# Kernel tuning notes

Hardware: AMD Instinct MI355X
Metric: run time of the kernel (lower is better)

The kernel has to match this reference:

```python
import jax, jax.numpy as jnp
import numpy as np

NUM_HEADS = 12
NUM_PATCHES = 4096
DIM = 768
IN_DIMS = DIM // NUM_HEADS
SCALE = NUM_PATCHES ** (-0.5)
LN_EPS = 1e-5


def setup_inputs() -> dict:
    key = jax.random.key(0)
    ks = jax.random.split(key, 14)
    s = 0.02
    return {
        "x": jax.random.normal(ks[0], (16, NUM_PATCHES, DIM), dtype=jnp.float32),
        "wq": jax.random.normal(ks[1], (DIM, DIM), dtype=jnp.float32) * s,
        "bq": jnp.zeros((DIM,), dtype=jnp.float32),
        "wk": jax.random.normal(ks[2], (DIM, DIM), dtype=jnp.float32) * s,
        "bk": jnp.zeros((DIM,), dtype=jnp.float32),
        "w_g": jax.random.normal(ks[3], (NUM_PATCHES,), dtype=jnp.float32),
        "w_fc": jax.random.normal(ks[4], (IN_DIMS, DIM), dtype=jnp.float32) * s,
        "b_fc": jnp.zeros((DIM,), dtype=jnp.float32),
        "w_fc2": jax.random.normal(ks[5], (NUM_HEADS, NUM_HEADS), dtype=jnp.float32) * s,
        "b_fc2": jnp.zeros((NUM_HEADS,), dtype=jnp.float32),
        "w_proj": jax.random.normal(ks[6], (DIM, DIM), dtype=jnp.float32) * s,
        "b_proj": jnp.zeros((DIM,), dtype=jnp.float32),
        "gamma": jnp.ones((DIM,), dtype=jnp.float32),
        "beta": jnp.zeros((DIM,), dtype=jnp.float32),
    }


def layernorm(x, gamma, beta):
    mu = jnp.mean(x, axis=-1, keepdims=True)
    var = jnp.mean(jnp.square(x - mu), axis=-1, keepdims=True)
    return (x - mu) * jax.lax.rsqrt(var + LN_EPS) * gamma + beta


def reference(x, wq, bq, wk, bk, w_g, w_fc, b_fc, w_fc2, b_fc2, w_proj, b_proj, gamma, beta):
    bs, n, d = x.shape
    q = x @ wq + bq                      # (b,n,d)  fc_q
    k = x @ wk + bk                      # (b,n,d)  fc_k (reassigned x in torch)
    # query_weight = (q^T @ w_g)^T -> (b,1,d); softmax over channel dim
    qw = jnp.einsum("bnd,n->bd", q, w_g) * SCALE
    A = jax.nn.softmax(qw, axis=-1)      # (b,d)
    # G = sum_n(A * k): A is constant over n, so equals A * sum_n k
    G = A * jnp.sum(k, axis=1)           # (b,d)
    # sigmoid gating chain on pooled q
    dv = jnp.mean(q, axis=1)             # (b,d)   AdaptiveAvgPool over n
    dv = dv.reshape(bs, NUM_HEADS, IN_DIMS)
    dv = jax.nn.gelu(dv @ w_fc + b_fc, approximate=False)   # (b,H,d)
    dv = dv.reshape(bs, d, NUM_HEADS)    # reshape (not transpose), as in torch
    dv = dv @ w_fc2 + b_fc2              # (b,d,H)
    dv = jax.nn.sigmoid(jnp.mean(dv, axis=-1))               # (b,d)
    G = G * dv                           # (b,d)
    out = (G[:, None, :] * k) @ w_proj + b_proj + layernorm(k, gamma, beta)
    return out
```

## Files before the change

### kernel.cpp

```cpp
#include <hip/hip_runtime.h>
#include <hip/hip_bf16.h>
#include <math.h>

#define NB 16
#define NP 4096
#define DDIM 768
#define MTOT (NB*NP)
#define N1 1536
#define SCALEF 0.015625f
#define LNEPS 1e-5f

typedef __attribute__((ext_vector_type(8))) short bf16x8;
typedef __attribute__((ext_vector_type(4))) float f32x4;
typedef __attribute__((ext_vector_type(4))) unsigned int u32x4;
typedef unsigned short us;

__device__ __forceinline__ us f2b(float f){
  union { float f; unsigned int u; } v; v.f = f;
  unsigned int u = v.u;
  unsigned int r = (u + 0x7FFFu + ((u >> 16) & 1u)) >> 16;
  return (us)r;
}
__device__ __forceinline__ unsigned int pack2(float a, float b){
  return (unsigned int)f2b(a) | ((unsigned int)f2b(b) << 16);
}
__device__ __forceinline__ float b2f(us h){
  union { unsigned int u; float f; } v; v.u = ((unsigned int)h) << 16;
  return v.f;
}
__device__ __forceinline__ float b2f_lo(unsigned int u){
  union { unsigned int x; float f; } v; v.x = u << 16; return v.f;
}
__device__ __forceinline__ float b2f_hi(unsigned int u){
  union { unsigned int x; float f; } v; v.x = u & 0xFFFF0000u; return v.f;
}

typedef __attribute__((address_space(1))) const unsigned int gas_u32;
typedef __attribute__((address_space(3))) unsigned int las_u32;
__device__ __forceinline__ void gl2lds16(const void* g, void* l){
  __builtin_amdgcn_global_load_lds((gas_u32*)g, (las_u32*)l, 16, 0, 0);
}

__global__ __launch_bounds__(256) void convert_x(const float* __restrict__ x,
                                                 us* __restrict__ xb){
  size_t i = ((size_t)blockIdx.x * 256 + threadIdx.x) * 8;
  const float4* s = reinterpret_cast<const float4*>(x + i);
  float4 a = s[0], b = s[1];
  u32x4 w;
  w[0] = pack2(a.x, a.y); w[1] = pack2(a.z, a.w);
  w[2] = pack2(b.x, b.y); w[3] = pack2(b.z, b.w);
  *reinterpret_cast<u32x4*>(xb + i) = w;
}

__global__ __launch_bounds__(256) void prep_w(const float* __restrict__ wq,
                                              const float* __restrict__ wk,
                                              const float* __restrict__ wp,
                                              us* __restrict__ wt1,
                                              us* __restrict__ wt2){
  int idx = blockIdx.x * 256 + threadIdx.x;
  const int tot1 = N1 * DDIM;
  if (idx < tot1){
    int n = idx / DDIM, k = idx % DDIM;
    float v = (n < DDIM) ? wq[k * DDIM + n] : wk[k * DDIM + (n - DDIM)];
    wt1[idx] = f2b(v);
  }
  int idx2 = idx - tot1;
  if (idx2 >= 0 && idx2 < DDIM * DDIM){
    int n = idx2 / DDIM, k = idx2 % DDIM;
    wt2[idx2] = f2b(wp[k * DDIM + n]);
  }
}

__global__ __launch_bounds__(256) void prep_wb(const us* __restrict__ wt2,
                                               const float* __restrict__ g,
                                               us* __restrict__ wbuf){
  size_t idx = (size_t)blockIdx.x * 256 + threadIdx.x;
  int d = (int)(idx % DDIM);
  size_t nd = idx / DDIM;
  int n = (int)(nd % DDIM);
  int b = (int)(nd / DDIM);
  float v = b2f(wt2[n * DDIM + d]) * g[(size_t)b * DDIM + d];
  wbuf[idx] = f2b(v);
}

__global__ __launch_bounds__(256) void ln_reduce(const float* __restrict__ lnS,
                                                 const float* __restrict__ lnQ,
                                                 float2* __restrict__ rstats){
  int r = blockIdx.x * 256 + threadIdx.x;
  float s = lnS[r] + lnS[MTOT + r] + lnS[2*MTOT + r];
  float q = lnQ[r] + lnQ[MTOT + r] + lnQ[2*MTOT + r];
  float mu = s * (1.0f / DDIM);
  float var = q * (1.0f / DDIM) - mu * mu;
  rstats[r] = make_float2(mu, rsqrtf(var + LNEPS));
}

__device__ __forceinline__ void gemm256_core(const us* __restrict__ Ag,
                                             const us* __restrict__ Bg,
                                             us* lds, int t,
                                             f32x4 (&acc)[4][4][2]){
  us* ldsA = lds;
  us* ldsB = lds + 32768;
  const int wave = t >> 6, lane = t & 63;
  const int wr = wave >> 2, wc = wave & 3, lr = lane & 15, lh = lane >> 4;
  const int srow = t >> 3;
  const int scell = (t & 7) ^ ((t >> 3) & 7);
  const int key8 = lane & 7;

  auto stage = [&](int sel, int h, int kt){
    const us* gb = sel ? Bg : Ag;
    us* lb = sel ? ldsB : ldsA;
    int slot = (2*kt + h) & 3;
    #pragma unroll
    for (int j = 0; j < 2; ++j){
      const us* src = gb + (size_t)(h*128 + j*64 + srow) * DDIM + kt*64 + scell*8;
      gl2lds16(src, lb + slot*8192 + j*4096 + (wave << 9));
    }
  };

  stage(0,0,0); stage(1,0,0); stage(1,1,0); stage(0,1,0);
  stage(0,0,1); stage(1,0,1); stage(1,1,1); stage(0,1,1);
  asm volatile("s_waitcnt vmcnt(8)" ::: "memory");
  __builtin_amdgcn_s_barrier();

  for (int kt = 0; kt < 12; ++kt){
    #pragma unroll
    for (int p = 0; p < 4; ++p){
      const int qm = p >> 1, qn = p & 1;
      const us* Ab = ldsA + ((2*kt + qm) & 3) * 8192;
      const us* Bb = ldsB + ((2*kt + qn) & 3) * 8192;
      bf16x8 av[4][2], bv[2][2];
      #pragma unroll
      for (int fm = 0; fm < 4; ++fm){
        int ra = wr*64 + fm*16 + lr;
        #pragma unroll
        for (int kk = 0; kk < 2; ++kk)
          av[fm][kk] = *reinterpret_cast<const bf16x8*>(
              &Ab[ra*64 + ((((kk<<2)|lh) ^ key8) << 3)]);
      }
      #pragma unroll
      for (int fn = 0; fn < 2; ++fn){
        int rb = wc*32 + fn*16 + lr;
        #pragma unroll
        for (int kk = 0; kk < 2; ++kk)
          bv[fn][kk] = *reinterpret_cast<const bf16x8*>(
              &Bb[rb*64 + ((((kk<<2)|lh) ^ key8) << 3)]);
      }
      if (kt >= 1 && kt <= 10){
        if      (p == 0) stage(0, 0, kt+1);
        else if (p == 1) stage(1, 0, kt+1);
        else if (p == 2) stage(1, 1, kt+1);
        else             stage(0, 1, kt+1);
      }
      __builtin_amdgcn_sched_barrier(0);
      __builtin_amdgcn_s_barrier();
      __builtin_amdgcn_s_setprio(1);
      #pragma unroll
      for (int fm = 0; fm < 4; ++fm)
        #pragma unroll
        for (int fn = 0; fn < 2; ++fn)
          #pragma unroll
          for (int kk = 0; kk < 2; ++kk)
            acc[p][fm][fn] = __builtin_amdgcn_mfma_f32_16x16x32_bf16(
                av[fm][kk], bv[fn][kk], acc[p][fm][fn], 0, 0, 0);
      __builtin_amdgcn_s_setprio(0);
      if (kt < 11)      { asm volatile("s_waitcnt vmcnt(4)" ::: "memory"); }
      else if (p == 0)  { asm volatile("s_waitcnt vmcnt(2)" ::: "memory"); }
      else if (p == 1)  { asm volatile("s_waitcnt vmcnt(0)" ::: "memory"); }
      __builtin_amdgcn_sched_barrier(0);
      __builtin_amdgcn_s_barrier();
    }
  }
}

__global__ __launch_bounds__(512, 2) void gemm_qk(
    const us* __restrict__ xb, const us* __restrict__ wt1,
    const float* __restrict__ bq, const float* __restrict__ bk,
    const float* __restrict__ w_g,
    us* __restrict__ kout,
    float* __restrict__ qwp, float* __restrict__ qsp, float* __restrict__ ksp,
    float* __restrict__ lnS, float* __restrict__ lnQ)
{
  extern __shared__ us lds[];
  int bid = blockIdx.x;
  int swz = (bid & 7) * ((int)gridDim.x >> 3) + (bid >> 3);
  int bn = swz % 6, bm = swz / 6;
  int m0 = bm * 256, n0 = bn * 256;
  int t = threadIdx.x;

  f32x4 acc[4][4][2] = {};
  gemm256_core(xb + (size_t)m0 * DDIM, wt1 + (size_t)n0 * DDIM, lds, t, acc);

  int wave = t >> 6, lane = t & 63;
  int wr = wave >> 2, wc = wave & 3, lr = lane & 15, lh = lane >> 4;
  bool is_q = (n0 < DDIM);
  int b = m0 >> 12, mc = (m0 & (NP-1)) >> 8;

  float bias[2][2];
  #pragma unroll
  for (int qn = 0; qn < 2; ++qn)
    #pragma unroll
    for (int fn = 0; fn < 2; ++fn){
      int col = qn*128 + wc*32 + fn*16 + lr;
      bias[qn][fn] = is_q ? bq[n0 + col] : bk[n0 - DDIM + col];
    }

  #pragma unroll
  for (int p = 0; p < 4; ++p){
    int qm = p >> 1, qn = p & 1;
    #pragma unroll
    for (int fm = 0; fm < 4; ++fm)
      #pragma unroll
      for (int r = 0; r < 4; ++r){
        int row = qm*128 + wr*64 + fm*16 + lh*4 + r;
        #pragma unroll
        for (int fn = 0; fn < 2; ++fn){
          int col = qn*128 + wc*32 + fn*16 + lr;
          lds[row*256 + (col ^ ((row & 7) << 3))] = f2b(acc[p][fm][fn][r] + bias[qn][fn]);
        }
      }
  }
  __syncthreads();

  int c8 = t & 31, rb = t >> 5;
  float cp[8] = {0,0,0,0,0,0,0,0};
  float cpw[8] = {0,0,0,0,0,0,0,0};
  float rs16[16], rq16[16];
  #pragma unroll
  for (int s = 0; s < 16; ++s){
    int row = s*16 + rb;
    u32x4 ch = *reinterpret_cast<const u32x4*>(&lds[row*256 + ((c8 ^ (row & 7)) << 3)]);
    float v[8];
    #pragma unroll
    for (int i = 0; i < 4; ++i){ v[2*i] = b2f_lo(ch[i]); v[2*i+1] = b2f_hi(ch[i]); }
    if (is_q){
      float wg = w_g[(m0 & (NP-1)) + row];
      #pragma unroll
      for (int j = 0; j < 8; ++j){ cp[j] += v[j]; cpw[j] += wg * v[j]; }
    } else {
      *reinterpret_cast<u32x4*>(kout + (size_t)(m0+row)*DDIM + (n0 - DDIM) + c8*8) = ch;
      float ss = 0.f, qq = 0.f;
      #pragma unroll
      for (int j = 0; j < 8; ++j){ cp[j] += v[j]; ss += v[j]; qq += v[j]*v[j]; }
      rs16[s] = ss; rq16[s] = qq;
    }
  }
  __syncthreads();
  float* colP  = reinterpret_cast<float*>(lds);
  float* colPw = colP + 4096;
  float* rowP  = colP + 8192;
  float* rowQ  = colP + 16384;
  #pragma unroll
  for (int j = 0; j < 8; ++j){
    colP[(c8*8+j)*16 + rb] = cp[j];
    if (is_q) colPw[(c8*8+j)*16 + rb] = cpw[j];
  }
  if (!is_q){
    #pragma unroll
    for (int s = 0; s < 16; ++s){
      int row = s*16 + rb;
      rowP[row*32 + c8] = rs16[s];
      rowQ[row*32 + c8] = rq16[s];
    }
  }
  __syncthreads();
  if (t < 256){
    float s0 = 0.f;
    #pragma unroll
    for (int i = 0; i < 16; ++i) s0 += colP[t*16 + i];
    size_t base = ((size_t)b * 16 + mc) * DDIM;
    if (is_q){
      float s1 = 0.f;
      #pragma unroll
      for (int i = 0; i < 16; ++i) s1 += colPw[t*16 + i];
      qwp[base + n0 + t] = s1;
      qsp[base + n0 + t] = s0;
    } else {
      ksp[base + (n0 - DDIM) + t] = s0;
      float rs_ = 0.f, rq_ = 0.f;
      #pragma unroll
      for (int i = 0; i < 32; ++i){ rs_ += rowP[t*32 + i]; rq_ += rowQ[t*32 + i]; }
      int kb = bn - 3;
      lnS[(size_t)kb * MTOT + m0 + t] = rs_;
      lnQ[(size_t)kb * MTOT + m0 + t] = rq_;
    }
  }
}

__global__ __launch_bounds__(256) void combine(
    const float* __restrict__ qwp, const float* __restrict__ qsp, const float* __restrict__ ksp,
    const float* __restrict__ w_fc, const float* __restrict__ b_fc,
    const float* __restrict__ w_fc2, const float* __restrict__ b_fc2,
    float* __restrict__ g)
{
  __shared__ float smA[DDIM];
  __shared__ float smQM[DDIM];
  __shared__ float smKS[DDIM];
  __shared__ float tmat[12][DDIM];
  __shared__ float red[256];
  __shared__ float wbar[12];
  __shared__ float bbar;
  int b = blockIdx.x, t = threadIdx.x;

  for (int col = t; col < DDIM; col += 256){
    float s0 = 0.f, s1 = 0.f, s2 = 0.f;
    for (int mc = 0; mc < 16; ++mc){
      size_t base = ((size_t)b * 16 + mc) * DDIM + col;
      s0 += qwp[base]; s1 += qsp[base]; s2 += ksp[base];
    }
    smA[col] = s0 * SCALEF;
    smQM[col] = s1 * (1.0f / NP);
    smKS[col] = s2;
  }
  __syncthreads();
  float lmax = -1e30f;
  for (int col = t; col < DDIM; col += 256) lmax = fmaxf(lmax, smA[col]);
  red[t] = lmax; __syncthreads();
  for (int off = 128; off; off >>= 1){
    if (t < off) red[t] = fmaxf(red[t], red[t + off]);
    __syncthreads();
  }
  float mx = red[0];
  __syncthreads();
  float lsum = 0.f;
  for (int col = t; col < DDIM; col += 256){
    float e = __expf(smA[col] - mx);
    smA[col] = e; lsum += e;
  }
  red[t] = lsum; __syncthreads();
  for (int off = 128; off; off >>= 1){
    if (t < off) red[t] += red[t + off];
    __syncthreads();
  }
  float inv = 1.0f / red[0];
  for (int col = t; col < DDIM; col += 256) smA[col] *= inv;

  if (t < 12){
    float s = 0.f;
    for (int j = 0; j < 12; ++j) s += w_fc2[t * 12 + j];
    wbar[t] = s * (1.0f / 12.0f);
  }
  if (t == 12){
    float s = 0.f;
    for (int j = 0; j < 12; ++j) s += b_fc2[j];
    bbar = s * (1.0f / 12.0f);
  }
  __syncthreads();
  for (int idx = t; idx < 12 * DDIM; idx += 256){
    int h = idx / DDIM, j = idx % DDIM;
    float s = b_fc[j];
    const float* qm = &smQM[h * 64];
    #pragma unroll 4
    for (int i = 0; i < 64; ++i) s += qm[i] * w_fc[i * DDIM + j];
    tmat[h][j] = 0.5f * s * (1.0f + erff(s * 0.70710678118654752f));
  }
  __syncthreads();
  for (int p = t; p < DDIM; p += 256){
    float s = bbar;
    #pragma unroll
    for (int m = 0; m < 12; ++m){
      int f = p * 12 + m;
      s += tmat[f / DDIM][f % DDIM] * wbar[m];
    }
    float dv = 1.0f / (1.0f + __expf(-s));
    g[(size_t)b * DDIM + p] = smA[p] * smKS[p] * dv;
  }
}

__global__ __launch_bounds__(512, 2) void gemm_out(
    const us* __restrict__ kin, const us* __restrict__ wbuf,
    const float2* __restrict__ rstats,
    const float* __restrict__ bp, const float* __restrict__ gamma,
    const float* __restrict__ beta,
    float* __restrict__ out)
{
  extern __shared__ us lds[];
  int bid = blockIdx.x;
  int swz = (bid & 7) * ((int)gridDim.x >> 3) + (bid >> 3);
  int bn = swz % 3, bm = swz / 3;
  int m0 = bm * 256, n0 = bn * 256;
  int t = threadIdx.x;
  int b = m0 >> 12;

  f32x4 acc[4][4][2] = {};
  gemm256_core(kin + (size_t)m0 * DDIM,
               wbuf + (size_t)b * DDIM * DDIM + (size_t)n0 * DDIM, lds, t, acc);

  int wave = t >> 6, lane = t & 63;
  int wr = wave >> 2, wc = wave & 3, lr = lane & 15, lh = lane >> 4;

  #pragma unroll
  for (int j = 0; j < 16; ++j){
    int row = j*16 + (t >> 5);
    const us* src = kin + (size_t)(m0 + row) * DDIM + n0 + (((t & 31) ^ (row & 7)) << 3);
    gl2lds16(src, lds + j*4096 + (wave << 9));
  }
  asm volatile("s_waitcnt vmcnt(0)" ::: "memory");
  __syncthreads();

  #pragma unroll
  for (int p = 0; p < 4; ++p){
    int qm = p >> 1, qn = p & 1;
    #pragma unroll
    for (int fn = 0; fn < 2; ++fn){
      int col = qn*128 + wc*32 + fn*16 + lr;
      float bpv = bp[n0 + col], gmv = gamma[n0 + col], btv = beta[n0 + col];
      #pragma unroll
      for (int fm = 0; fm < 4; ++fm)
        #pragma unroll
        for (int r = 0; r < 4; ++r){
          int row = qm*128 + wr*64 + fm*16 + lh*4 + r;
          float2 st = rstats[m0 + row];
          float kv = b2f(lds[row*256 + (col ^ ((row & 7) << 3))]);
          acc[p][fm][fn][r] += bpv + (kv - st.x) * st.y * gmv + btv;
        }
    }
  }
  __syncthreads();

  float* fb = reinterpret_cast<float*>(lds);
  #pragma unroll
  for (int h = 0; h < 2; ++h){
    #pragma unroll
    for (int qm2 = 0; qm2 < 2; ++qm2){
      int p = qm2*2 + h;
      #pragma unroll
      for (int fm = 0; fm < 4; ++fm)
        #pragma unroll
        for (int r = 0; r < 4; ++r){
          int row = qm2*128 + wr*64 + fm*16 + lh*4 + r;
          #pragma unroll
          for (int fn = 0; fn < 2; ++fn){
            int c = wc*32 + fn*16 + lr;
            fb[row*128 + (c ^ ((row & 7) << 2))] = acc[p][fm][fn][r];
          }
        }
    }
    __syncthreads();
    #pragma unroll
    for (int s = 0; s < 16; ++s){
      int u = s*512 + t;
      int row = u >> 5, c4 = u & 31;
      float4 vv = *reinterpret_cast<const float4*>(&fb[row*128 + ((c4 ^ (row & 7)) << 2)]);
      *reinterpret_cast<float4*>(&out[(size_t)(m0 + row) * DDIM + n0 + h*128 + c4*4]) = vv;
    }
    __syncthreads();
  }
}

extern "C" void kernel_launch(void* const* d_in, const int* in_sizes, int n_in,
                              void* d_out, int out_size, void* d_ws, size_t ws_size,
                              hipStream_t stream)
{
  const float* x      = (const float*)d_in[0];
  const float* wq     = (const float*)d_in[1];
  const float* bq     = (const float*)d_in[2];
  const float* wk     = (const float*)d_in[3];
  const float* bk     = (const float*)d_in[4];
  const float* w_g    = (const float*)d_in[5];
  const float* w_fc   = (const float*)d_in[6];
  const float* b_fc   = (const float*)d_in[7];
  const float* w_fc2  = (const float*)d_in[8];
  const float* b_fc2  = (const float*)d_in[9];
  const float* w_proj = (const float*)d_in[10];
  const float* b_proj = (const float*)d_in[11];
  const float* gamma  = (const float*)d_in[12];
  const float* beta   = (const float*)d_in[13];
  float* out = (float*)d_out;

  char* ws = (char*)d_ws;
  us*     xb    = (us*)(ws);
  us*     kbuf  = (us*)(ws + 100663296);
  us*     wt1   = (us*)(ws + 201326592);
  us*     wt2   = (us*)(ws + 203685888);
  us*     wbuf  = (us*)(ws + 204865536);
  float*  qwp   = (float*)(ws + 223739904);
  float*  qsp   = (float*)(ws + 224526336);
  float*  ksp   = (float*)(ws + 225312768);
  float*  lnS   = (float*)(ws + 226099200);
  float*  lnQ   = (float*)(ws + 226885632);
  float*  g     = (float*)(ws + 227672064);
  float2* rstat = (float2*)(ws + 227721216);

  convert_x<<<dim3(MTOT * DDIM / (256 * 8)), dim3(256), 0, stream>>>(x, xb);
  prep_w<<<dim3((N1 * DDIM + DDIM * DDIM) / 256), dim3(256), 0, stream>>>(wq, wk, w_proj, wt1, wt2);
  gemm_qk<<<dim3((MTOT / 256) * (N1 / 256)), dim3(512), 131072, stream>>>(
      xb, wt1, bq, bk, w_g, kbuf, qwp, qsp, ksp, lnS, lnQ);
  ln_reduce<<<dim3(MTOT / 256), dim3(256), 0, stream>>>(lnS, lnQ, rstat);
  combine<<<dim3(NB), dim3(256), 0, stream>>>(qwp, qsp, ksp, w_fc, b_fc, w_fc2, b_fc2, g);
  prep_wb<<<dim3(NB * DDIM * DDIM / 256), dim3(256), 0, stream>>>(wt2, g, wbuf);
  gemm_out<<<dim3((MTOT / 256) * (DDIM / 256)), dim3(512), 131072, stream>>>(
      kbuf, wbuf, rstat, b_proj, gamma, beta, out);
}
```

Before: 535.4 us.

## Replace quadrant-staged GEMM pipeline with simple double-buffered full-tile prefetch

Replaces the 4-slot, per-quadrant staged LDS pipeline in the 256x256 GEMM core with a simple double buffer. Each k-step now issues loads for the whole next A and B tile and waits on all of them with vmcnt(0), with one barrier per k-step. B fragments are held for both column halves so A fragments are reused across two MFMA chains. This cuts barrier count and keeps more MFMAs in flight per load phase. In exchange it drops the fine-grained overlap and the setprio hints, and the register pressure from holding extra B fragments could hurt occupancy.

```diff
diff --git a/kernel.cpp b/kernel.cpp
--- a/kernel.cpp
+++ b/kernel.cpp
@@ -106,70 +106,87 @@
   const int scell = (t & 7) ^ ((t >> 3) & 7);
   const int key8 = lane & 7;
 
-  auto stage = [&](int sel, int h, int kt){
-    const us* gb = sel ? Bg : Ag;
-    us* lb = sel ? ldsB : ldsA;
-    int slot = (2*kt + h) & 3;
-    #pragma unroll
-    for (int j = 0; j < 2; ++j){
-      const us* src = gb + (size_t)(h*128 + j*64 + srow) * DDIM + kt*64 + scell*8;
-      gl2lds16(src, lb + slot*8192 + j*4096 + (wave << 9));
+  auto stage_all = [&](int kt){
+    int pb = (kt & 1) << 14;
+    #pragma unroll
+    for (int j = 0; j < 4; ++j){
+      const us* sa = Ag + (size_t)(j*64 + srow) * DDIM + kt*64 + scell*8;
+      gl2lds16(sa, ldsA + pb + j*4096 + (wave << 9));
+    }
+    #pragma unroll
+    for (int j = 0; j < 4; ++j){
+      const us* sb = Bg + (size_t)(j*64 + srow) * DDIM + kt*64 + scell*8;
+      gl2lds16(sb, ldsB + pb + j*4096 + (wave << 9));
     }
   };
 
-  stage(0,0,0); stage(1,0,0); stage(1,1,0); stage(0,1,0);
-  stage(0,0,1); stage(1,0,1); stage(1,1,1); stage(0,1,1);
-  asm volatile("s_waitcnt vmcnt(8)" ::: "memory");
+  stage_all(0);
+
+  bf16x8 av[4][2], bv0[2][2], bv1[2][2];
+
+  for (int kt = 0; kt < 12; ++kt){
+    asm volatile("s_waitcnt vmcnt(0)" ::: "memory");
+    __builtin_amdgcn_sched_barrier(0);
+    __builtin_amdgcn_s_barrier();
+    if (kt < 11) stage_all(kt + 1);
+
+    const int pb = (kt & 1) << 14;
+    const us* Ab = ldsA + pb;
+    const us* Bb = ldsB + pb;
+
+    #pragma unroll
+    for (int fm = 0; fm < 4; ++fm){
+      int ra = 0*128 + wr*64 + fm*16 + lr;
+      #pragma unroll
+      for (int kk = 0; kk < 2; ++kk)
+        av[fm][kk] = *reinterpret_cast<const bf16x8*>(
+            &Ab[ra*64 + ((((kk<<2)|lh) ^ key8) << 3)]);
+    }
+    #pragma unroll
+    for (int fn = 0; fn < 2; ++fn){
+      int rb0 = 0*128 + wc*32 + fn*16 + lr;
+      int rb1 = 1*128 + wc*32 + fn*16 + lr;
+      #pragma unroll
+      for (int kk = 0; kk < 2; ++kk){
+        bv0[fn][kk] = *reinterpret_cast<const bf16x8*>(
+            &Bb[rb0*64 + ((((kk<<2)|lh) ^ key8) << 3)]);
+        bv1[fn][kk] = *reinterpret_cast<const bf16x8*>(
+            &Bb[rb1*64 + ((((kk<<2)|lh) ^ key8) << 3)]);
+      }
+    }
+    #pragma unroll
+    for (int fm = 0; fm < 4; ++fm)
+      #pragma unroll
+      for (int fn = 0; fn < 2; ++fn)
+        #pragma unroll
+        for (int kk = 0; kk < 2; ++kk){
+          acc[0][fm][fn] = __builtin_amdgcn_mfma_f32_16x16x32_bf16(
+              av[fm][kk], bv0[fn][kk], acc[0][fm][fn], 0, 0, 0);
+          acc[1][fm][fn] = __builtin_amdgcn_mfma_f32_16x16x32_bf16(
+              av[fm][kk], bv1[fn][kk], acc[1][fm][fn], 0, 0, 0);
+        }
+
+    #pragma unroll
+    for (int fm = 0; fm < 4; ++fm){
+      int ra = 1*128 + wr*64 + fm*16 + lr;
+      #pragma unroll
+      for (int kk = 0; kk < 2; ++kk)
+        av[fm][kk] = *reinterpret_cast<const bf16x8*>(
+            &Ab[ra*64 + ((((kk<<2)|lh) ^ key8) << 3)]);
+    }
+    #pragma unroll
+    for (int fm = 0; fm < 4; ++fm)
+      #pragma unroll
+      for (int fn = 0; fn < 2; ++fn)
+        #pragma unroll
+        for (int kk = 0; kk < 2; ++kk){
+          acc[2][fm][fn] = __builtin_amdgcn_mfma_f32_16x16x32_bf16(
+              av[fm][kk], bv0[fn][kk], acc[2][fm][fn], 0, 0, 0);
+          acc[3][fm][fn] = __builtin_amdgcn_mfma_f32_16x16x32_bf16(
+              av[fm][kk], bv1[fn][kk], acc[3][fm][fn], 0, 0, 0);
+        }
+  }
   __builtin_amdgcn_s_barrier();
-
-  for (int kt = 0; kt < 12; ++kt){
-    #pragma unroll
-    for (int p = 0; p < 4; ++p){
-      const int qm = p >> 1, qn = p & 1;
-      const us* Ab = ldsA + ((2*kt + qm) & 3) * 8192;
-      const us* Bb = ldsB + ((2*kt + qn) & 3) * 8192;
-      bf16x8 av[4][2], bv[2][2];
-      #pragma unroll
-      for (int fm = 0; fm < 4; ++fm){
-        int ra = wr*64 + fm*16 + lr;
-        #pragma unroll
-        for (int kk = 0; kk < 2; ++kk)
-          av[fm][kk] = *reinterpret_cast<const bf16x8*>(
-              &Ab[ra*64 + ((((kk<<2)|lh) ^ key8) << 3)]);
-      }
-      #pragma unroll
-      for (int fn = 0; fn < 2; ++fn){
-        int rb = wc*32 + fn*16 + lr;
-        #pragma unroll
-        for (int kk = 0; kk < 2; ++kk)
-          bv[fn][kk] = *reinterpret_cast<const bf16x8*>(
-              &Bb[rb*64 + ((((kk<<2)|lh) ^ key8) << 3)]);
-      }
-      if (kt >= 1 && kt <= 10){
-        if      (p == 0) stage(0, 0, kt+1);
-        else if (p == 1) stage(1, 0, kt+1);
-        else if (p == 2) stage(1, 1, kt+1);
-        else             stage(0, 1, kt+1);
-      }
-      __builtin_amdgcn_sched_barrier(0);
-      __builtin_amdgcn_s_barrier();
-      __builtin_amdgcn_s_setprio(1);
-      #pragma unroll
-      for (int fm = 0; fm < 4; ++fm)
-        #pragma unroll
-        for (int fn = 0; fn < 2; ++fn)
-          #pragma unroll
-          for (int kk = 0; kk < 2; ++kk)
-            acc[p][fm][fn] = __builtin_amdgcn_mfma_f32_16x16x32_bf16(
-                av[fm][kk], bv[fn][kk], acc[p][fm][fn], 0, 0, 0);
-      __builtin_amdgcn_s_setprio(0);
-      if (kt < 11)      { asm volatile("s_waitcnt vmcnt(4)" ::: "memory"); }
-      else if (p == 0)  { asm volatile("s_waitcnt vmcnt(2)" ::: "memory"); }
-      else if (p == 1)  { asm volatile("s_waitcnt vmcnt(0)" ::: "memory"); }
-      __builtin_amdgcn_sched_barrier(0);
-      __builtin_amdgcn_s_barrier();
-    }
-  }
 }
 
 __global__ __launch_bounds__(512, 2) void gemm_qk(
```

Result: faster. 524.9 us (-2.0%).
